# Kernel tuning notes

Hardware: AMD Instinct MI355X
Metric: run time of the kernel (lower is better)

## Reference

```python
import jax, jax.numpy as jnp
import numpy as np

PH, PW, SP, C, FH, FW = 7, 7, 4, 10, 34, 34
STRIDE = 8.0


def setup_inputs() -> dict:
    key = jax.random.key(0)
    k1, k2, k3, k4, k5 = jax.random.split(key, 5)
    ft = jax.random.normal(k1, (1, C * PH * PW, FH, FW), dtype=jnp.float32)
    N = 10000
    # rois: (batch_idx, x1, y1, x2, y2) in image coords (im ~ 270x270)
    x1 = jax.random.uniform(k2, (N,), dtype=jnp.float32) * 240.0
    y1 = jax.random.uniform(k3, (N,), dtype=jnp.float32) * 240.0
    w = 8.0 + jax.random.uniform(k4, (N,), dtype=jnp.float32) * 80.0
    h = 8.0 + jax.random.uniform(k5, (N,), dtype=jnp.float32) * 80.0
    rois = jnp.stack([jnp.zeros((N,), jnp.float32), x1, y1,
                      jnp.minimum(x1 + w, 269.0), jnp.minimum(y1 + h, 269.0)], axis=1)
    return {"ft_add_left_right": ft, "rois": rois}


def reference(ft_add_left_right, rois):
    N = rois.shape[0]
    # [PH, PW, FH, FW, C] position-sensitive feature map
    feat = jnp.transpose(ft_add_left_right[0].reshape(C, PH, PW, FH, FW), (1, 2, 3, 4, 0))

    rsw = rois[:, 1] / STRIDE
    rsh = rois[:, 2] / STRIDE
    rew = rois[:, 3] / STRIDE
    reh = rois[:, 4] / STRIDE
    roi_h = jnp.where(reh - rsh > 0.1, reh - rsh, 0.1)  # torch.threshold(x, 0.1, 0.1)
    roi_w = jnp.where(rew - rsw > 0.1, rew - rsw, 0.1)
    bin_h, bin_w = roi_h / PH, roi_w / PW
    sub_h, sub_w = bin_h / SP, bin_w / SP

    pidx = jnp.arange(PH, dtype=jnp.float32)
    sidx = jnp.arange(SP, dtype=jnp.float32) + 0.5
    # sample coords: h [N, PH, SP], w [N, PW, SP]
    hstart = jnp.floor(rsh[:, None] + pidx[None, :] * bin_h[:, None])
    wstart = jnp.floor(rsw[:, None] + pidx[None, :] * bin_w[:, None])
    h = hstart[:, :, None] + sidx[None, None, :] * sub_h[:, None, None]
    w = wstart[:, :, None] + sidx[None, None, :] * sub_w[:, None, None]

    # broadcast to [N, PH, PW, SP(h), SP(w)]
    Hc = h[:, :, None, :, None]
    Wc = w[:, None, :, None, :]
    keep = (Wc > -1) & (Wc < FW) & (Hc > -1) & (Hc < FH)  # [N,PH,PW,SP,SP]

    x1f, y1f = jnp.floor(Wc), jnp.floor(Hc)
    x2f, y2f = jnp.ceil(Wc), jnp.ceil(Hc)
    dx, dy = Wc - x1f, Hc - y1f
    x1, x2 = x1f.astype(jnp.int32), x2f.astype(jnp.int32)
    y1, y2 = y1f.astype(jnp.int32), y2f.astype(jnp.int32)
    x1v, x2v = (x1 >= 0) & (x1 < FW), (x2 >= 0) & (x2 < FW)
    y1v, y2v = (y1 >= 0) & (y1 < FH), (y2 >= 0) & (y2 < FH)
    x1c, x2c = jnp.clip(x1, 0, FW - 1), jnp.clip(x2, 0, FW - 1)
    y1c, y2c = jnp.clip(y1, 0, FH - 1), jnp.clip(y2, 0, FH - 1)

    phidx = jnp.arange(PH)[None, :, None, None, None]
    pwidx = jnp.arange(PW)[None, None, :, None, None]

    def corner(yi, xi, valid, wgt):
        v = feat[phidx, pwidx, yi, xi]  # [N,PH,PW,SP,SP,C]
        m = (wgt * valid.astype(wgt.dtype))
        return v * m[..., None]

    value = (corner(y1c, x1c, x1v & y1v, (1 - dx) * (1 - dy))
             + corner(y2c, x1c, x1v & y2v, (1 - dx) * dy)
             + corner(y1c, x2c, x2v & y1v, dx * (1 - dy))
             + corner(y2c, x2c, x2v & y2v, dx * dy))
    keep_f = keep.astype(value.dtype)
    sum_ = jnp.sum(value * keep_f[..., None], axis=(3, 4))  # [N,PH,PW,C]
    count = jnp.sum(keep_f, axis=(3, 4))                    # [N,PH,PW]
    result = jnp.where(count[..., None] > 0, sum_ / jnp.maximum(count, 1.0)[..., None], 0.0)
    # bins ordered ph*PW + pw -> [N, C, 49]
    return jnp.transpose(result.reshape(N, PH * PW, C), (0, 2, 1))
```

## Files before the change

### kernel.cpp

```cpp
#include <hip/hip_runtime.h>

#define PH 7
#define PW 7
#define SP 4
#define C 10
#define FH 34
#define FW 34
#define NBIN (PH*PW)
#define PLANE (FH*FW)
#define NP (NBIN*PLANE)
#define RPB 1024
#define NOUTC (C*NBIN)
#define NR (NOUTC/2)
#define TJ 16

typedef float nf4 __attribute__((ext_vector_type(4)));
typedef __fp16 h2v __attribute__((ext_vector_type(2)));

__device__ __forceinline__ unsigned int pk_h2(float a, float b) {
    h2v h = __builtin_amdgcn_cvt_pkrtz(a, b);
    return *(unsigned int*)&h;
}
__device__ __forceinline__ float2 up_h2(unsigned int u) {
    h2v h = *(h2v*)&u;
    return make_float2((float)h.x, (float)h.y);
}

__device__ __forceinline__ unsigned int pack_bf2(float lo, float hi) {
    unsigned int a = __float_as_uint(lo);
    a += 0x7FFFu + ((a >> 16) & 1u);
    unsigned int b = __float_as_uint(hi);
    b += 0x7FFFu + ((b >> 16) & 1u);
    return (a >> 16) | (b & 0xFFFF0000u);
}
__device__ __forceinline__ float bf2f_lo(unsigned int u) {
    return __uint_as_float(u << 16);
}
__device__ __forceinline__ float bf2f_hi(unsigned int u) {
    return __uint_as_float(u & 0xFFFF0000u);
}

struct AxisW { float w0, w1, w2; int base; };

__device__ __forceinline__ AxisW axis_weights_fast(float rs, float re, int p, int F) {
#pragma clang fp contract(off)
    float d  = re - rs;
    float sp = (d > 0.1f) ? d : 0.1f;
    float bs = sp / 7.0f;
    float ss = bs / 4.0f;
    float st = floorf(rs + (float)p * bs);
    int   B0 = (int)st;

    float w0 = 0.f, w1 = 0.f, w2 = 0.f;
#pragma unroll
    for (int s = 0; s < SP; ++s) {
        float v  = st + ((float)s + 0.5f) * ss;
        float f1 = floorf(v);
        float dv = v - f1;
        int   i1 = (int)f1;
        float a  = 1.0f - dv;
        float b  = (i1 + 1 < F) ? dv : 0.0f;
        bool  z  = (i1 == B0);
        w0 += z ? a : 0.0f;
        w1 += z ? b : a;
        w2 += z ? 0.0f : b;
    }
    w0 *= 0.25f; w1 *= 0.25f; w2 *= 0.25f;

    int Bc = min(B0, F - 3);
    int dB = B0 - Bc;
    AxisW out;
    out.w0 = (dB == 0) ? w0 : 0.0f;
    out.w1 = (dB == 0) ? w1 : (dB == 1) ? w0 : 0.0f;
    out.w2 = (dB == 0) ? w2 : (dB == 1) ? w1 : w0;
    out.base = Bc;
    return out;
}

__device__ __forceinline__ AxisW axis_weights(float rs, float re, int p, int F) {
#pragma clang fp contract(off)
    float d  = re - rs;
    float sp = (d > 0.1f) ? d : 0.1f;
    float bs = sp / 7.0f;
    float ss = bs / 4.0f;
    float st = floorf(rs + (float)p * bs);
    int   B0 = (int)floorf(st);

    float w0 = 0.f, w1 = 0.f, w2 = 0.f; int cnt = 0;
#pragma unroll
    for (int s = 0; s < SP; ++s) {
        float v = st + ((float)s + 0.5f) * ss;
        if (v > -1.0f && v < (float)F) {
            ++cnt;
            float f1 = floorf(v);
            float dv = v - f1;
            int   i1 = (int)f1;
            int   i2 = (int)ceilf(v);
            float a  = (1.0f - dv) * ((i1 >= 0 && i1 < F) ? 1.0f : 0.0f);
            float b  = dv          * ((i2 >= 0 && i2 < F) ? 1.0f : 0.0f);
            int o1 = i1 - B0;
            int o2 = i2 - B0;
            w0 += (o1 == 0) ? a : 0.0f;
            w1 += (o1 == 1) ? a : 0.0f;
            w1 += (o2 == 1) ? b : 0.0f;
            w2 += (o2 == 2) ? b : 0.0f;
        }
    }
    float rc = (cnt > 0) ? 1.0f / (float)cnt : 0.0f;
    w0 *= rc; w1 *= rc; w2 *= rc;

    int Bc = min(max(B0, 0), F - 3);
    int dB = B0 - Bc;
    int m0 = 0 - dB, m1 = 1 - dB, m2 = 2 - dB;
    AxisW out;
    out.w0 = (m0 == 0) ? w0 : (m0 == 1) ? w1 : (m0 == 2) ? w2 : 0.0f;
    out.w1 = (m1 == 0) ? w0 : (m1 == 1) ? w1 : (m1 == 2) ? w2 : 0.0f;
    out.w2 = (m2 == 0) ? w0 : (m2 == 1) ? w1 : (m2 == 2) ? w2 : 0.0f;
    out.base = Bc;
    return out;
}

__global__ __launch_bounds__(RPB, 8) void roi_kernel(const float* __restrict__ ft,
                                                     const float* __restrict__ rois,
                                                     unsigned int* __restrict__ ws2,
                                                     int N, int blocksPerBin,
                                                     int tiled) {
    __shared__ __align__(16) unsigned int ldsA[PLANE * 4];
    __shared__ unsigned int ldsB[PLANE];

    const int bin   = blockIdx.x / blocksPerBin;
    const int chunk = blockIdx.x % blocksPerBin;
    const int tid   = threadIdx.x;
    const int ph    = bin / PW;
    const int pw    = bin % PW;

    const int n = chunk * RPB + tid;
    const int nv = (n < N) ? n : 0;
    const float* r = rois + nv * 5;
    float rx1 = r[1] * 0.125f;
    float ry1 = r[2] * 0.125f;
    float rx2 = r[3] * 0.125f;
    float ry2 = r[4] * 0.125f;

    {
        const float* fb = ft + (size_t)bin * PLANE;
        for (int pix = tid; pix < PLANE; pix += RPB) {
            float c0 = fb[pix];
            float c1 = fb[NP + pix];
            float c2 = fb[2 * (size_t)NP + pix];
            float c3 = fb[3 * (size_t)NP + pix];
            float c4 = fb[4 * (size_t)NP + pix];
            float c5 = fb[5 * (size_t)NP + pix];
            float c6 = fb[6 * (size_t)NP + pix];
            float c7 = fb[7 * (size_t)NP + pix];
            uint4 v;
            v.x = pk_h2(c0, c1);
            v.y = pk_h2(c2, c3);
            v.z = pk_h2(c4, c5);
            v.w = pk_h2(c6, c7);
            *(uint4*)&ldsA[pix * 4] = v;
            float c8 = fb[8 * (size_t)NP + pix];
            float c9 = fb[9 * (size_t)NP + pix];
            ldsB[pix] = pk_h2(c8, c9);
        }
    }

    AxisW H = axis_weights_fast(ry1, ry2, ph, FH);
    AxisW W = axis_weights_fast(rx1, rx2, pw, FW);
    const int wbase = H.base * FW + W.base;
    float rw[3] = {H.w0, H.w1, H.w2};
    float cw[3] = {W.w0, W.w1, W.w2};

    __syncthreads();

    if (n >= N) return;

    float a0 = 0.f, a1 = 0.f, a2 = 0.f, a3 = 0.f, a4 = 0.f;
    float a5 = 0.f, a6 = 0.f, a7 = 0.f, a8 = 0.f, a9 = 0.f;
#pragma unroll
    for (int j = 0; j < 3; ++j) {
        float wy = rw[j];
#pragma unroll
        for (int i = 0; i < 3; ++i) {
            float w = wy * cw[i];
            int pix = wbase + j * FW + i;
            uint4 pA = *(const uint4*)&ldsA[pix * 4];
            unsigned int pB = ldsB[pix];
            float2 f01 = up_h2(pA.x);
            float2 f23 = up_h2(pA.y);
            float2 f45 = up_h2(pA.z);
            float2 f67 = up_h2(pA.w);
            float2 f89 = up_h2(pB);
            a0 += w * f01.x; a1 += w * f01.y;
            a2 += w * f23.x; a3 += w * f23.y;
            a4 += w * f45.x; a5 += w * f45.y;
            a6 += w * f67.x; a7 += w * f67.y;
            a8 += w * f89.x; a9 += w * f89.y;
        }
    }

    unsigned int* o;
    size_t ks;
    if (tiled) {
        o  = ws2 + (size_t)(n >> 4) * (NR * TJ) + (size_t)(bin * 5) * TJ + (n & 15);
        ks = TJ;
    } else {
        o  = ws2 + (size_t)(bin * 5) * N + n;
        ks = N;
    }
    o[0 * ks] = pack_bf2(a0, a1);
    o[1 * ks] = pack_bf2(a2, a3);
    o[2 * ks] = pack_bf2(a4, a5);
    o[3 * ks] = pack_bf2(a6, a7);
    o[4 * ks] = pack_bf2(a8, a9);
}

__global__ __launch_bounds__(256) void transpose_out(const unsigned int* __restrict__ ws2,
                                                     float* __restrict__ out, int N,
                                                     int tiled) {
    __shared__ __align__(16) float t[TJ * NOUTC];
    int n0  = blockIdx.x * TJ;
    int tid = threadIdx.x;
    bool fastLin = !tiled && (n0 + TJ <= N) && ((N & 3) == 0);

    if (tiled) {
        const unsigned int* wt = ws2 + (size_t)blockIdx.x * (NR * TJ);
        for (int idx = tid; idx < NR * 4; idx += 256) {
            uint4 v = *(const uint4*)(wt + idx * 4);
            int r = idx >> 2;
            int q = idx & 3;
            int bin  = r / 5;
            int k    = r - bin * 5;
            int col0 = (2 * k) * NBIN + bin;
            float* tb = &t[(q * 4) * NOUTC + col0];
            tb[0 * NOUTC]        = bf2f_lo(v.x);
            tb[0 * NOUTC + NBIN] = bf2f_hi(v.x);
            tb[1 * NOUTC]        = bf2f_lo(v.y);
            tb[1 * NOUTC + NBIN] = bf2f_hi(v.y);
            tb[2 * NOUTC]        = bf2f_lo(v.z);
            tb[2 * NOUTC + NBIN] = bf2f_hi(v.z);
            tb[3 * NOUTC]        = bf2f_lo(v.w);
            tb[3 * NOUTC + NBIN] = bf2f_hi(v.w);
        }
    } else if (fastLin) {
        for (int idx = tid; idx < NR * 4; idx += 256) {
            int r = idx >> 2;
            int q = idx & 3;
            uint4 v = *(const uint4*)(ws2 + (size_t)r * N + n0 + q * 4);
            int bin  = r / 5;
            int k    = r - bin * 5;
            int col0 = (2 * k) * NBIN + bin;
            float* tb = &t[(q * 4) * NOUTC + col0];
            tb[0 * NOUTC]        = bf2f_lo(v.x);
            tb[0 * NOUTC + NBIN] = bf2f_hi(v.x);
            tb[1 * NOUTC]        = bf2f_lo(v.y);
            tb[1 * NOUTC + NBIN] = bf2f_hi(v.y);
            tb[2 * NOUTC]        = bf2f_lo(v.z);
            tb[2 * NOUTC + NBIN] = bf2f_hi(v.z);
            tb[3 * NOUTC]        = bf2f_lo(v.w);
            tb[3 * NOUTC + NBIN] = bf2f_hi(v.w);
        }
    } else {
        for (int idx = tid; idx < NR * TJ; idx += 256) {
            int r = idx / TJ;
            int j = idx - r * TJ;
            int n = n0 + j;
            unsigned int v = (n < N) ? ws2[(size_t)r * N + n] : 0u;
            int bin  = r / 5;
            int k    = r - bin * 5;
            int col0 = (2 * k) * NBIN + bin;
            t[j * NOUTC + col0]        = bf2f_lo(v);
            t[j * NOUTC + col0 + NBIN] = bf2f_hi(v);
        }
    }
    __syncthreads();

    if (tiled || fastLin) {
        const nf4* t4  = (const nf4*)t;
        nf4* out4 = (nf4*)(out + (size_t)n0 * NOUTC);
        for (int idx = tid; idx < TJ * NOUTC / 4; idx += 256)
            __builtin_nontemporal_store(t4[idx], &out4[idx]);
    } else {
        for (int idx = tid; idx < TJ * NOUTC; idx += 256) {
            int j   = idx / NOUTC;
            int col = idx - j * NOUTC;
            int n   = n0 + j;
            if (n < N) out[(size_t)n * NOUTC + col] = t[j * NOUTC + col];
        }
    }
}

__global__ __launch_bounds__(256) void roi_direct(const float* __restrict__ ft,
                                                  const float* __restrict__ rois,
                                                  float* __restrict__ out, int N) {
#pragma clang fp contract(off)
    int tid = blockIdx.x * blockDim.x + threadIdx.x;
    if (tid >= N * NBIN) return;
    int bin = tid % NBIN;
    int n   = tid / NBIN;
    int ph  = bin / PW;
    int pw  = bin % PW;
    const float* r = rois + n * 5;
    float rsw = r[1]*0.125f, rsh = r[2]*0.125f, rew = r[3]*0.125f, reh = r[4]*0.125f;
    AxisW H = axis_weights(rsh, reh, ph, FH);
    AxisW W = axis_weights(rsw, rew, pw, FW);
    float rw[3] = {H.w0, H.w1, H.w2};
    float cw[3] = {W.w0, W.w1, W.w2};
    float acc[C];
    for (int c = 0; c < C; ++c) acc[c] = 0.0f;
    const float* base = ft + (size_t)bin * PLANE;
    for (int j = 0; j < 3; ++j) {
        int y = H.base + j;
        for (int i = 0; i < 3; ++i) {
            int x = W.base + i;
            float w = rw[j] * cw[i];
            int off = y * FW + x;
            for (int c = 0; c < C; ++c)
                acc[c] += w * base[(size_t)c * NP + off];
        }
    }
    float* o = out + (size_t)n * NOUTC + bin;
    for (int c = 0; c < C; ++c) o[c * NBIN] = acc[c];
}

extern "C" void kernel_launch(void* const* d_in, const int* in_sizes, int n_in,
                              void* d_out, int out_size, void* d_ws, size_t ws_size,
                              hipStream_t stream) {
    const float* ft   = (const float*)d_in[0];
    const float* rois = (const float*)d_in[1];
    float* out = (float*)d_out;
    int N = in_sizes[1] / 5;

    size_t need = (size_t)NR * N * sizeof(unsigned int);

    if (ws_size >= need) {
        unsigned int* ws2 = (unsigned int*)d_ws;
        int tiled = (N % TJ == 0) ? 1 : 0;
        int blocksPerBin = (N + RPB - 1) / RPB;
        roi_kernel<<<NBIN * blocksPerBin, RPB, 0, stream>>>(ft, rois, ws2,
                                                            N, blocksPerBin, tiled);
        int tblocks = (N + TJ - 1) / TJ;
        transpose_out<<<tblocks, 256, 0, stream>>>(ws2, out, N, tiled);
    } else {
        int total = N * NBIN;
        roi_direct<<<(total + 255) / 256, 256, 0, stream>>>(ft, rois, out, N);
    }
}
```

Baseline: 73.58 us.

## Pre-pack feature planes to fp16 once in a separate kernel

Adds a pack_ft kernel that converts each bin's 10-channel fp32 plane into a contiguous fp16 record in workspace, done once per bin rather than once per ROI block. The main ROI kernel then fills LDS with contiguous uint4 copies of that record instead of ten strided fp32 gathers plus conversion. This removes the repeated conversion work across the roughly ten blocks per bin. The cost is an extra kernel launch and a global round-trip through workspace.

```diff
diff --git a/kernel.cpp b/kernel.cpp
--- a/kernel.cpp
+++ b/kernel.cpp
@@ -13,6 +13,9 @@
 #define NOUTC (C*NBIN)
 #define NR (NOUTC/2)
 #define TJ 16
+#define RECW  (PLANE*5)
+#define REC4  (PLANE*5/4)
+#define RECPADW 5792
 
 typedef float nf4 __attribute__((ext_vector_type(4)));
 typedef __fp16 h2v __attribute__((ext_vector_type(2)));
@@ -120,13 +123,39 @@
     return out;
 }
 
-__global__ __launch_bounds__(RPB, 8) void roi_kernel(const float* __restrict__ ft,
+__global__ __launch_bounds__(256) void pack_ft(const float* __restrict__ ft,
+                                               unsigned int* __restrict__ pf) {
+    const int bin = blockIdx.x;
+    const float* fb = ft + (size_t)bin * PLANE;
+    unsigned int* pa = pf + (size_t)bin * RECPADW;
+    unsigned int* pb = pa + PLANE * 4;
+    for (int pix = threadIdx.x; pix < PLANE; pix += 256) {
+        float c0 = fb[pix];
+        float c1 = fb[NP + pix];
+        float c2 = fb[2 * (size_t)NP + pix];
+        float c3 = fb[3 * (size_t)NP + pix];
+        float c4 = fb[4 * (size_t)NP + pix];
+        float c5 = fb[5 * (size_t)NP + pix];
+        float c6 = fb[6 * (size_t)NP + pix];
+        float c7 = fb[7 * (size_t)NP + pix];
+        float c8 = fb[8 * (size_t)NP + pix];
+        float c9 = fb[9 * (size_t)NP + pix];
+        uint4 v;
+        v.x = pk_h2(c0, c1);
+        v.y = pk_h2(c2, c3);
+        v.z = pk_h2(c4, c5);
+        v.w = pk_h2(c6, c7);
+        *(uint4*)&pa[pix * 4] = v;
+        pb[pix] = pk_h2(c8, c9);
+    }
+}
+
+__global__ __launch_bounds__(RPB, 8) void roi_kernel(const unsigned int* __restrict__ pf,
                                                      const float* __restrict__ rois,
                                                      unsigned int* __restrict__ ws2,
                                                      int N, int blocksPerBin,
                                                      int tiled) {
-    __shared__ __align__(16) unsigned int ldsA[PLANE * 4];
-    __shared__ unsigned int ldsB[PLANE];
+    __shared__ __align__(16) unsigned int ldsw[RECW];
 
     const int bin   = blockIdx.x / blocksPerBin;
     const int chunk = blockIdx.x % blocksPerBin;
@@ -143,26 +172,11 @@
     float ry2 = r[4] * 0.125f;
 
     {
-        const float* fb = ft + (size_t)bin * PLANE;
-        for (int pix = tid; pix < PLANE; pix += RPB) {
-            float c0 = fb[pix];
-            float c1 = fb[NP + pix];
-            float c2 = fb[2 * (size_t)NP + pix];
-            float c3 = fb[3 * (size_t)NP + pix];
-            float c4 = fb[4 * (size_t)NP + pix];
-            float c5 = fb[5 * (size_t)NP + pix];
-            float c6 = fb[6 * (size_t)NP + pix];
-            float c7 = fb[7 * (size_t)NP + pix];
-            uint4 v;
-            v.x = pk_h2(c0, c1);
-            v.y = pk_h2(c2, c3);
-            v.z = pk_h2(c4, c5);
-            v.w = pk_h2(c6, c7);
-            *(uint4*)&ldsA[pix * 4] = v;
-            float c8 = fb[8 * (size_t)NP + pix];
-            float c9 = fb[9 * (size_t)NP + pix];
-            ldsB[pix] = pk_h2(c8, c9);
-        }
+        const uint4* pfb = (const uint4*)(pf + (size_t)bin * RECPADW);
+        uint4* l4 = (uint4*)ldsw;
+        l4[tid] = pfb[tid];
+        if (tid < REC4 - RPB)
+            l4[tid + RPB] = pfb[tid + RPB];
     }
 
     AxisW H = axis_weights_fast(ry1, ry2, ph, FH);
@@ -184,8 +198,8 @@
         for (int i = 0; i < 3; ++i) {
             float w = wy * cw[i];
             int pix = wbase + j * FW + i;
-            uint4 pA = *(const uint4*)&ldsA[pix * 4];
-            unsigned int pB = ldsB[pix];
+            uint4 pA = *(const uint4*)&ldsw[pix * 4];
+            unsigned int pB = ldsw[PLANE * 4 + pix];
             float2 f01 = up_h2(pA.x);
             float2 f23 = up_h2(pA.y);
             float2 f45 = up_h2(pA.z);
@@ -331,13 +345,16 @@
     float* out = (float*)d_out;
     int N = in_sizes[1] / 5;
 
-    size_t need = (size_t)NR * N * sizeof(unsigned int);
+    size_t ws2_words = ((size_t)NR * N + 3) & ~(size_t)3;
+    size_t need = (ws2_words + (size_t)NBIN * RECPADW) * sizeof(unsigned int);
 
     if (ws_size >= need) {
         unsigned int* ws2 = (unsigned int*)d_ws;
+        unsigned int* pf  = ws2 + ws2_words;
         int tiled = (N % TJ == 0) ? 1 : 0;
         int blocksPerBin = (N + RPB - 1) / RPB;
-        roi_kernel<<<NBIN * blocksPerBin, RPB, 0, stream>>>(ft, rois, ws2,
+        pack_ft<<<NBIN, 256, 0, stream>>>(ft, pf);
+        roi_kernel<<<NBIN * blocksPerBin, RPB, 0, stream>>>(pf, rois, ws2,
                                                             N, blocksPerBin, tiled);
         int tblocks = (N + TJ - 1) / TJ;
         transpose_out<<<tblocks, 256, 0, stream>>>(ws2, out, N, tiled);
```

After: 77.73 us. 1.06x slower.
